# Kernel optimization log

Hardware: AMD Instinct MI355X
Metric: run time of the kernel (lower is better)

## Reference

```python
import jax, jax.numpy as jnp
import numpy as np
from jax import lax

B, T, IN, H, NCLASS = 256, 512, 64, 128, 6
SCALE = 0.05


def setup_inputs() -> dict:
    key = jax.random.key(0)
    ks = jax.random.split(key, 9)
    return {
        "x": jax.random.normal(ks[0], (B, T, IN), jnp.float32),
        "w_ih0": jax.random.normal(ks[1], (3 * H, IN), jnp.float32) * SCALE,
        "w_ih1": jax.random.normal(ks[2], (3 * H, H), jnp.float32) * SCALE,
        "w_ih2": jax.random.normal(ks[3], (3 * H, H), jnp.float32) * SCALE,
        "w_hh": jax.random.normal(ks[4], (3, 3 * H, H), jnp.float32) * SCALE,
        "b_ih": jax.random.normal(ks[5], (3, 3 * H), jnp.float32) * SCALE,
        "b_hh": jax.random.normal(ks[6], (3, 3 * H), jnp.float32) * SCALE,
        "fc_w": jax.random.normal(ks[7], (NCLASS, H), jnp.float32) * SCALE,
        "fc_b": jax.random.normal(ks[8], (NCLASS,), jnp.float32) * SCALE,
    }


def _gru_layer(x, w_ih, w_hh, b_ih, b_hh):
    # x: [B, T, in]; PyTorch gate order: r, z, n
    gx = jnp.einsum("bti,gi->btg", x, w_ih) + b_ih          # [B, T, 3H]
    gx_r, gx_z, gx_n = jnp.split(gx, 3, axis=-1)
    w_hr, w_hz, w_hn = jnp.split(w_hh, 3, axis=0)           # each [H, H]
    b_hr, b_hz, b_hn = jnp.split(b_hh, 3)

    def step(h, g):
        gr, gz, gn = g
        r = jax.nn.sigmoid(gr + h @ w_hr.T + b_hr)
        z = jax.nn.sigmoid(gz + h @ w_hz.T + b_hz)
        n = jnp.tanh(gn + r * (h @ w_hn.T + b_hn))
        h_new = (1.0 - z) * n + z * h
        return h_new, h_new

    h0 = jnp.zeros((x.shape[0], w_hh.shape[1]), x.dtype)
    xs = (gx_r.transpose(1, 0, 2), gx_z.transpose(1, 0, 2), gx_n.transpose(1, 0, 2))
    _, hs = lax.scan(step, h0, xs)                          # hs: [T, B, H]
    return hs.transpose(1, 0, 2)                            # [B, T, H]


def reference(x, w_ih0, w_ih1, w_ih2, w_hh, b_ih, b_hh, fc_w, fc_b):
    h = _gru_layer(x, w_ih0, w_hh[0], b_ih[0], b_hh[0])
    h = _gru_layer(h, w_ih1, w_hh[1], b_ih[1], b_hh[1])
    h = _gru_layer(h, w_ih2, w_hh[2], b_ih[2], b_hh[2])
    last = h[:, -1, :]                                      # [B, H]
    # Dropout2d(0.25) is identity in eval mode.
    return last @ fc_w.T + fc_b                             # [B, NCLASS]
```

## Files before the change

### kernel.cpp

```cpp
#include <hip/hip_runtime.h>
#include <stdint.h>


#define B_   256
#define T_   512
#define IN_  64
#define H_   128
#define G_   384

typedef short bf16x8 __attribute__((ext_vector_type(8)));
typedef float f32x4  __attribute__((ext_vector_type(4)));

__device__ __forceinline__ unsigned short f2bf(float f) {
  union { float f; unsigned u; } v; v.f = f;
  unsigned u = v.u;
  u += 0x7fffu + ((u >> 16) & 1u);
  return (unsigned short)(u >> 16);
}
__device__ __forceinline__ float bf2f(unsigned short h) {
  union { unsigned u; float f; } v; v.u = ((unsigned)h) << 16; return v.f;
}

template <int K, bool AF32>
__global__ __launch_bounds__(512) void gemm_gx(const void* __restrict__ Ap,
                                               const float* __restrict__ W,
                                               unsigned short* __restrict__ gx) {
  __shared__ __align__(16) unsigned short lA[128 * K];
  __shared__ __align__(16) unsigned short lW[G_ * K];
  const int tid = threadIdx.x;
  const int m0 = blockIdx.x * 128;

  if (AF32) {
    const float* A = (const float*)Ap;
    const int nch = 128 * K / 4;
    for (int c = tid; c < nch; c += 512) {
      int row = c / (K / 4), kq = c - row * (K / 4);
      float4 v = *(const float4*)(A + (size_t)(m0 + row) * K + kq * 4);
      unsigned long long pk = (unsigned long long)f2bf(v.x) |
                              ((unsigned long long)f2bf(v.y) << 16) |
                              ((unsigned long long)f2bf(v.z) << 32) |
                              ((unsigned long long)f2bf(v.w) << 48);
      unsigned byte = ((unsigned)(row * K + kq * 4) * 2u) ^ (((unsigned)row & 7u) << 4);
      *(unsigned long long*)((char*)lA + byte) = pk;
    }
  } else {
    const unsigned short* A = (const unsigned short*)Ap;
    const int nch = 128 * K / 8;
    for (int c = tid; c < nch; c += 512) {
      int row = c / (K / 8), ko = c - row * (K / 8);
      bf16x8 v = *(const bf16x8*)(A + (size_t)(m0 + row) * K + ko * 8);
      unsigned byte = ((unsigned)(row * K + ko * 8) * 2u) ^ (((unsigned)row & 7u) << 4);
      *(bf16x8*)((char*)lA + byte) = v;
    }
  }
  {
    const int nch = G_ * K / 4;
    for (int c = tid; c < nch; c += 512) {
      int g = c / (K / 4), kq = c - g * (K / 4);
      float4 v = *(const float4*)(W + (size_t)g * K + kq * 4);
      unsigned long long pk = (unsigned long long)f2bf(v.x) |
                              ((unsigned long long)f2bf(v.y) << 16) |
                              ((unsigned long long)f2bf(v.z) << 32) |
                              ((unsigned long long)f2bf(v.w) << 48);
      unsigned byte = ((unsigned)(g * K + kq * 4) * 2u) ^ (((unsigned)g & 7u) << 4);
      *(unsigned long long*)((char*)lW + byte) = pk;
    }
  }
  __syncthreads();

  const int l = tid & 63, w = tid >> 6;
  const int rg = w >> 2, cg = w & 3;
  const int lr = l & 15, g4 = l >> 4;

  f32x4 acc[4][6];
#pragma unroll
  for (int i = 0; i < 4; ++i)
#pragma unroll
    for (int j = 0; j < 6; ++j) acc[i][j] = (f32x4){0.f, 0.f, 0.f, 0.f};

#pragma unroll
  for (int ks = 0; ks < K / 32; ++ks) {
    bf16x8 a[4];
#pragma unroll
    for (int i = 0; i < 4; ++i) {
      int row = (rg * 4 + i) * 16 + lr;
      unsigned byte = ((unsigned)(row * K + ks * 32 + g4 * 8) * 2u) ^ (((unsigned)row & 7u) << 4);
      a[i] = *(const bf16x8*)((const char*)lA + byte);
    }
#pragma unroll
    for (int j = 0; j < 6; ++j) {
      int g = (cg * 6 + j) * 16 + lr;
      unsigned byte = ((unsigned)(g * K + ks * 32 + g4 * 8) * 2u) ^ (((unsigned)g & 7u) << 4);
      bf16x8 bfr = *(const bf16x8*)((const char*)lW + byte);
#pragma unroll
      for (int i = 0; i < 4; ++i)
        acc[i][j] = __builtin_amdgcn_mfma_f32_16x16x32_bf16(a[i], bfr, acc[i][j], 0, 0, 0);
    }
  }

#pragma unroll
  for (int i = 0; i < 4; ++i)
#pragma unroll
    for (int j = 0; j < 6; ++j)
#pragma unroll
      for (int r = 0; r < 4; ++r) {
        int m = m0 + (rg * 4 + i) * 16 + g4 * 4 + r;
        int g = (cg * 6 + j) * 16 + lr;
        int t, b;
        if (AF32) { t = m & 511; b = m >> 9; } else { t = m >> 8; b = m & 255; }
        gx[(size_t)(t * 256 + b) * G_ + g] = f2bf(acc[i][j][r]);
      }
}

template <int DOSEQ, int DOFC>
__global__ __launch_bounds__(512) void gru_scan(
    const unsigned short* __restrict__ gx,
    const float* __restrict__ Whh,
    const float* __restrict__ bih,
    const float* __restrict__ bhh,
    unsigned short* __restrict__ hseq,
    const float* __restrict__ fcw,
    const float* __restrict__ fcb,
    float* __restrict__ out) {
  __shared__ __align__(16) unsigned short lh[2][2048];
  __shared__ __align__(16) unsigned short lgx[2][1536];

  const int tid = threadIdx.x, l = tid & 63, w = tid >> 6;
  const int lr = l & 15, g4 = l >> 4;
  const int b0 = blockIdx.x * 4;
  const int batch = g4;
  const int hcol = w * 16 + lr;

  for (int i = tid; i < 4096; i += 512) ((unsigned short*)lh)[i] = 0;

  const float c_r  = bih[hcol]           + bhh[hcol];
  const float c_z  = bih[128 + hcol]     + bhh[128 + hcol];
  const float c_n1 = bih[256 + hcol];
  const float c_n2 = bhh[256 + hcol];

  bf16x8 Bf[3][4];
#pragma unroll
  for (int ci = 0; ci < 3; ++ci) {
    int gcol = (w + ci * 8) * 16 + lr;
#pragma unroll
    for (int ks = 0; ks < 4; ++ks) {
      const float* p = Whh + (size_t)gcol * H_ + ks * 32 + g4 * 8;
      float4 v0 = *(const float4*)p;
      float4 v1 = *(const float4*)(p + 4);
      bf16x8 f;
      f[0] = (short)f2bf(v0.x); f[1] = (short)f2bf(v0.y);
      f[2] = (short)f2bf(v0.z); f[3] = (short)f2bf(v0.w);
      f[4] = (short)f2bf(v1.x); f[5] = (short)f2bf(v1.y);
      f[6] = (short)f2bf(v1.z); f[7] = (short)f2bf(v1.w);
      Bf[ci][ks] = f;
    }
  }

  const bool pfa = tid < 384;
  if (pfa) {
    unsigned long long v =
        *(const unsigned long long*)((const char*)gx + (size_t)b0 * G_ * 2 + tid * 8);
    *(unsigned long long*)((char*)&lgx[0][0] + tid * 8) = v;
  }
  __syncthreads();

  float hreg = 0.f;

  for (int t = 0; t < T_; ++t) {
    const int cur = t & 1, nxt = cur ^ 1;
    const int tp1 = (t + 1 < T_) ? t + 1 : (T_ - 1);

    unsigned long long pfv = 0;
    if (pfa)
      pfv = *(const unsigned long long*)((const char*)gx +
            ((size_t)(tp1 * 256 + b0) * G_) * 2 + tid * 8);

    bf16x8 a[4];
#pragma unroll
    for (int ks = 0; ks < 4; ++ks) {
      unsigned byte = ((unsigned)(lr * 256 + ks * 64 + g4 * 16)) ^ (((unsigned)lr & 7u) << 4);
      a[ks] = *(const bf16x8*)((const char*)lh[cur] + byte);
    }

    f32x4 aR = (f32x4){0.f, 0.f, 0.f, 0.f};
    f32x4 aZ = (f32x4){0.f, 0.f, 0.f, 0.f};
    f32x4 aN = (f32x4){0.f, 0.f, 0.f, 0.f};
#pragma unroll
    for (int ks = 0; ks < 4; ++ks) {
      aR = __builtin_amdgcn_mfma_f32_16x16x32_bf16(a[ks], Bf[0][ks], aR, 0, 0, 0);
      aZ = __builtin_amdgcn_mfma_f32_16x16x32_bf16(a[ks], Bf[1][ks], aZ, 0, 0, 0);
      aN = __builtin_amdgcn_mfma_f32_16x16x32_bf16(a[ks], Bf[2][ks], aN, 0, 0, 0);
    }

    float hWr, hWz, hWn;
    {
      float y0 = __shfl(aR[0], lr, 64), y1 = __shfl(aR[1], lr, 64);
      float y2 = __shfl(aR[2], lr, 64), y3 = __shfl(aR[3], lr, 64);
      hWr = batch == 0 ? y0 : batch == 1 ? y1 : batch == 2 ? y2 : y3;
    }
    {
      float y0 = __shfl(aZ[0], lr, 64), y1 = __shfl(aZ[1], lr, 64);
      float y2 = __shfl(aZ[2], lr, 64), y3 = __shfl(aZ[3], lr, 64);
      hWz = batch == 0 ? y0 : batch == 1 ? y1 : batch == 2 ? y2 : y3;
    }
    {
      float y0 = __shfl(aN[0], lr, 64), y1 = __shfl(aN[1], lr, 64);
      float y2 = __shfl(aN[2], lr, 64), y3 = __shfl(aN[3], lr, 64);
      hWn = batch == 0 ? y0 : batch == 1 ? y1 : batch == 2 ? y2 : y3;
    }

    const float gxr = bf2f(lgx[cur][batch * G_ + hcol]);
    const float gxz = bf2f(lgx[cur][batch * G_ + 128 + hcol]);
    const float gxn = bf2f(lgx[cur][batch * G_ + 256 + hcol]);

    const float rg = 1.f / (1.f + __expf(-(gxr + hWr + c_r)));
    const float zg = 1.f / (1.f + __expf(-(gxz + hWz + c_z)));
    const float nx = gxn + c_n1 + rg * (hWn + c_n2);
    const float ng = 1.f - 2.f / (__expf(2.f * nx) + 1.f);
    hreg = (1.f - zg) * ng + zg * hreg;

    const unsigned short hb = f2bf(hreg);
    *(unsigned short*)((char*)lh[nxt] +
        (((unsigned)(batch * 256 + hcol * 2)) ^ ((unsigned)batch << 4))) = hb;
    if (DOSEQ)
      hseq[(size_t)(t * 256 + b0 + batch) * H_ + hcol] = hb;

    if (pfa) *(unsigned long long*)((char*)&lgx[nxt][0] + tid * 8) = pfv;

    __syncthreads();
  }

  if (DOFC) {
    float* sc = (float*)&lgx[0][0];
    sc[batch * H_ + hcol] = hreg;
    __syncthreads();
    if (tid < 24) {
      int b = tid / 6, c = tid - b * 6;
      float s = fcb[c];
      for (int k = 0; k < H_; ++k) s += sc[b * H_ + k] * fcw[c * H_ + k];
      out[(size_t)(b0 + b) * 6 + c] = s;
    }
  }
}

extern "C" void kernel_launch(void* const* d_in, const int* in_sizes, int n_in,
                              void* d_out, int out_size, void* d_ws, size_t ws_size,
                              hipStream_t stream) {
  const float* x     = (const float*)d_in[0];
  const float* w_ih0 = (const float*)d_in[1];
  const float* w_ih1 = (const float*)d_in[2];
  const float* w_ih2 = (const float*)d_in[3];
  const float* w_hh  = (const float*)d_in[4];
  const float* b_ih  = (const float*)d_in[5];
  const float* b_hh  = (const float*)d_in[6];
  const float* fc_w  = (const float*)d_in[7];
  const float* fc_b  = (const float*)d_in[8];
  float* out = (float*)d_out;

  unsigned short* gxb  = (unsigned short*)d_ws;
  unsigned short* hseq = gxb + (size_t)T_ * B_ * G_;

  gemm_gx<64, true><<<1024, 512, 0, stream>>>((const void*)x, w_ih0, gxb);
  gru_scan<1, 0><<<64, 512, 0, stream>>>(gxb, w_hh, b_ih, b_hh, hseq,
                                         nullptr, nullptr, nullptr);
  gemm_gx<128, false><<<1024, 512, 0, stream>>>((const void*)hseq, w_ih1, gxb);
  gru_scan<1, 0><<<64, 512, 0, stream>>>(gxb, w_hh + 1 * G_ * H_, b_ih + G_,
                                         b_hh + G_, hseq, nullptr, nullptr, nullptr);
  gemm_gx<128, false><<<1024, 512, 0, stream>>>((const void*)hseq, w_ih2, gxb);
  gru_scan<0, 1><<<64, 512, 0, stream>>>(gxb, w_hh + 2 * G_ * H_, b_ih + 2 * G_,
                                         b_hh + 2 * G_, nullptr, fc_w, fc_b, out);
}
```

Measured before the change: 1.334 ms.

## Prefetch gate inputs three steps ahead via direct-to-LDS loads; stage GEMM stores

The GRU scan now keeps a four-slot LDS ring of precomputed input gates. Three waves issue asynchronous global-to-LDS loads three timesteps ahead and wait with explicit vmcnt counters plus raw barriers. This replaces the one-step register prefetch that sat on the serial recurrence path. The input-projection GEMM also stages its output tile through shared memory so it can write coalesced 16-byte rows instead of scattered 2-byte stores. The hand-tuned waitcnt values depend on exactly how many memory ops are in flight, which makes the code fragile.

```diff
diff --git a/kernel.cpp b/kernel.cpp
--- a/kernel.cpp
+++ b/kernel.cpp
@@ -10,6 +10,7 @@
 
 typedef short bf16x8 __attribute__((ext_vector_type(8)));
 typedef float f32x4  __attribute__((ext_vector_type(4)));
+typedef unsigned long long u64x2 __attribute__((ext_vector_type(2)));
 
 __device__ __forceinline__ unsigned short f2bf(float f) {
   union { float f; unsigned u; } v; v.f = f;
@@ -21,12 +22,19 @@
   union { unsigned u; float f; } v; v.u = ((unsigned)h) << 16; return v.f;
 }
 
+__device__ __forceinline__ void gload16(const void* g, void* l) {
+  __builtin_amdgcn_global_load_lds(
+      (const __attribute__((address_space(1))) void*)g,
+      (__attribute__((address_space(3))) void*)l, 16, 0, 0);
+}
+
 template <int K, bool AF32>
 __global__ __launch_bounds__(512) void gemm_gx(const void* __restrict__ Ap,
                                                const float* __restrict__ W,
                                                unsigned short* __restrict__ gx) {
-  __shared__ __align__(16) unsigned short lA[128 * K];
-  __shared__ __align__(16) unsigned short lW[G_ * K];
+  __shared__ __align__(16) unsigned short smem[(128 + G_) * K];
+  unsigned short* lA = smem;
+  unsigned short* lW = smem + 128 * K;
   const int tid = threadIdx.x;
   const int m0 = blockIdx.x * 128;
 
@@ -98,18 +106,38 @@
     }
   }
 
-#pragma unroll
-  for (int i = 0; i < 4; ++i)
-#pragma unroll
-    for (int j = 0; j < 6; ++j)
-#pragma unroll
-      for (int r = 0; r < 4; ++r) {
-        int m = m0 + (rg * 4 + i) * 16 + g4 * 4 + r;
-        int g = (cg * 6 + j) * 16 + lr;
-        int t, b;
-        if (AF32) { t = m & 511; b = m >> 9; } else { t = m >> 8; b = m & 255; }
-        gx[(size_t)(t * 256 + b) * G_ + g] = f2bf(acc[i][j][r]);
-      }
+  unsigned short* lC = smem;
+#pragma unroll
+  for (int half = 0; half < 2; ++half) {
+    __syncthreads();
+    if (rg == half) {
+#pragma unroll
+      for (int i = 0; i < 4; ++i)
+#pragma unroll
+        for (int j = 0; j < 6; ++j)
+#pragma unroll
+          for (int r = 0; r < 4; ++r) {
+            int mloc = i * 16 + g4 * 4 + r;
+            int g = (cg * 6 + j) * 16 + lr;
+            lC[mloc * 388 + g] = f2bf(acc[i][j][r]);
+          }
+    }
+    __syncthreads();
+    for (int it = 0; it < 6; ++it) {
+      int c = tid + it * 512;
+      int mloc = c / 48, cb = c - mloc * 48;
+      unsigned long long lo =
+          *(const unsigned long long*)((const char*)lC + mloc * 776 + cb * 16);
+      unsigned long long hi =
+          *(const unsigned long long*)((const char*)lC + mloc * 776 + cb * 16 + 8);
+      int m = m0 + half * 64 + mloc;
+      int row;
+      if (AF32) { int t = m & 511, b = m >> 9; row = t * 256 + b; }
+      else      { row = m; }
+      u64x2 v; v[0] = lo; v[1] = hi;
+      *(u64x2*)((char*)gx + (size_t)row * (G_ * 2) + cb * 16) = v;
+    }
+  }
 }
 
 template <int DOSEQ, int DOFC>
@@ -123,7 +151,7 @@
     const float* __restrict__ fcb,
     float* __restrict__ out) {
   __shared__ __align__(16) unsigned short lh[2][2048];
-  __shared__ __align__(16) unsigned short lgx[2][1536];
+  __shared__ __align__(16) unsigned short lgx[4][1536];
 
   const int tid = threadIdx.x, l = tid & 63, w = tid >> 6;
   const int lr = l & 15, g4 = l >> 4;
@@ -156,24 +184,24 @@
     }
   }
 
-  const bool pfa = tid < 384;
-  if (pfa) {
-    unsigned long long v =
-        *(const unsigned long long*)((const char*)gx + (size_t)b0 * G_ * 2 + tid * 8);
-    *(unsigned long long*)((char*)&lgx[0][0] + tid * 8) = v;
-  }
   __syncthreads();
+  if (w < 3) {
+#pragma unroll
+    for (int p = 0; p < 3; ++p) {
+      const char* src = (const char*)gx + ((size_t)(p * 256 + b0) * G_) * 2 + (size_t)tid * 16;
+      gload16(src, (char*)&lgx[p][0] + w * 1024);
+    }
+    asm volatile("s_waitcnt vmcnt(2)" ::: "memory");
+  }
+  asm volatile("s_waitcnt lgkmcnt(0)" ::: "memory");
+  __builtin_amdgcn_s_barrier();
+  __builtin_amdgcn_sched_barrier(0);
 
   float hreg = 0.f;
 
   for (int t = 0; t < T_; ++t) {
     const int cur = t & 1, nxt = cur ^ 1;
-    const int tp1 = (t + 1 < T_) ? t + 1 : (T_ - 1);
-
-    unsigned long long pfv = 0;
-    if (pfa)
-      pfv = *(const unsigned long long*)((const char*)gx +
-            ((size_t)(tp1 * 256 + b0) * G_) * 2 + tid * 8);
+    const int slot = t & 3;
 
     bf16x8 a[4];
 #pragma unroll
@@ -181,6 +209,9 @@
       unsigned byte = ((unsigned)(lr * 256 + ks * 64 + g4 * 16)) ^ (((unsigned)lr & 7u) << 4);
       a[ks] = *(const bf16x8*)((const char*)lh[cur] + byte);
     }
+    const float gxr = bf2f(lgx[slot][batch * G_ + hcol]);
+    const float gxz = bf2f(lgx[slot][batch * G_ + 128 + hcol]);
+    const float gxn = bf2f(lgx[slot][batch * G_ + 256 + hcol]);
 
     f32x4 aR = (f32x4){0.f, 0.f, 0.f, 0.f};
     f32x4 aZ = (f32x4){0.f, 0.f, 0.f, 0.f};
@@ -209,10 +240,6 @@
       hWn = batch == 0 ? y0 : batch == 1 ? y1 : batch == 2 ? y2 : y3;
     }
 
-    const float gxr = bf2f(lgx[cur][batch * G_ + hcol]);
-    const float gxz = bf2f(lgx[cur][batch * G_ + 128 + hcol]);
-    const float gxn = bf2f(lgx[cur][batch * G_ + 256 + hcol]);
-
     const float rg = 1.f / (1.f + __expf(-(gxr + hWr + c_r)));
     const float zg = 1.f / (1.f + __expf(-(gxz + hWz + c_z)));
     const float nx = gxn + c_n1 + rg * (hWn + c_n2);
@@ -225,12 +252,23 @@
     if (DOSEQ)
       hseq[(size_t)(t * 256 + b0 + batch) * H_ + hcol] = hb;
 
-    if (pfa) *(unsigned long long*)((char*)&lgx[nxt][0] + tid * 8) = pfv;
-
+    if (w < 3) {
+      int t3 = t + 3; if (t3 > T_ - 1) t3 = T_ - 1;
+      const char* src = (const char*)gx + ((size_t)(t3 * 256 + b0) * G_) * 2 + (size_t)tid * 16;
+      gload16(src, (char*)&lgx[(t + 3) & 3][0] + w * 1024);
+    }
+
+    __builtin_amdgcn_sched_barrier(0);
+    if (w < 3) {
+      asm volatile("s_waitcnt vmcnt(%0)" :: "n"(DOSEQ ? 3 : 2) : "memory");
+    }
+    asm volatile("s_waitcnt lgkmcnt(0)" ::: "memory");
+    __builtin_amdgcn_s_barrier();
+    __builtin_amdgcn_sched_barrier(0);
+  }
+
+  if (DOFC) {
     __syncthreads();
-  }
-
-  if (DOFC) {
     float* sc = (float*)&lgx[0][0];
     sc[batch * H_ + hcol] = hreg;
     __syncthreads();
```

Result: no change. 1.330 ms (-0.3%).
